# Performance work log

Hardware: AMD Instinct MI355X
Metric: run time of the kernel (lower is better)

## Reference

```python
import jax, jax.numpy as jnp
import numpy as np

EPS = 1e-5
N_HEADS = 8

def _layernorm(h, g, b):
    mu = jnp.mean(h, axis=-1, keepdims=True)
    var = jnp.mean((h - mu) ** 2, axis=-1, keepdims=True)
    return g * (h - mu) * jax.lax.rsqrt(var + EPS) + b

def _mlp_ln(x, W1, b1, W2, b2, g, beta):
    # Linear -> SiLU -> Linear -> LayerNorm (torch nn.Sequential processor)
    h = jax.nn.silu(x @ W1.T + b1)
    h = h @ W2.T + b2
    return _layernorm(h, g, beta)

def setup_inputs() -> dict:
    key = jax.random.key(0)
    ks = jax.random.split(key, 16)
    B, S, D = 4, 2048, 1024
    M, P, C = 128, 256, 512
    def lin(k, o, i):
        return (jax.random.normal(k, (o, i), jnp.float32) / np.sqrt(i)).astype(jnp.float32)
    inp = {}
    inp['x'] = jax.random.normal(ks[0], (B, S, D), jnp.float32)
    inp['scale_types'] = jax.random.randint(ks[1], (B, S), 0, 3)
    for name, dim, k1, k2 in [('mol', M, 2, 3), ('path', P, 4, 5), ('cell', C, 6, 7)]:
        inp[name + '_W1'] = lin(ks[k1], dim, D)
        inp[name + '_b1'] = jnp.zeros((dim,), jnp.float32)
        inp[name + '_W2'] = lin(ks[k2], dim, dim)
        inp[name + '_b2'] = jnp.zeros((dim,), jnp.float32)
        inp[name + '_g'] = jnp.ones((dim,), jnp.float32)
        inp[name + '_beta'] = jnp.zeros((dim,), jnp.float32)
    inp['int_W1'] = lin(ks[8], D, M + P + C)
    inp['int_b1'] = jnp.zeros((D,), jnp.float32)
    inp['int_W2'] = lin(ks[9], D, D)
    inp['int_b2'] = jnp.zeros((D,), jnp.float32)
    inp['int_g'] = jnp.ones((D,), jnp.float32)
    inp['int_beta'] = jnp.zeros((D,), jnp.float32)
    inp['attn_Wqkv'] = lin(ks[10], 3 * D, D)
    inp['attn_bqkv'] = jnp.zeros((3 * D,), jnp.float32)
    inp['attn_Wo'] = lin(ks[11], D, D)
    inp['attn_bo'] = jnp.zeros((D,), jnp.float32)
    inp['scale_w'] = jnp.ones((3,), jnp.float32) / 3.0
    return inp

def reference(x, scale_types,
              mol_W1, mol_b1, mol_W2, mol_b2, mol_g, mol_beta,
              path_W1, path_b1, path_W2, path_b2, path_g, path_beta,
              cell_W1, cell_b1, cell_W2, cell_b2, cell_g, cell_beta,
              int_W1, int_b1, int_W2, int_b2, int_g, int_beta,
              attn_Wqkv, attn_bqkv, attn_Wo, attn_bo, scale_w):
    B, S, D = x.shape
    # per-token routing: each token goes through exactly one expert; the
    # other two scale outputs are zeros (mask instead of Python loop).
    mol = _mlp_ln(x, mol_W1, mol_b1, mol_W2, mol_b2, mol_g, mol_beta) * (scale_types == 0)[..., None]
    path = _mlp_ln(x, path_W1, path_b1, path_W2, path_b2, path_g, path_beta) * (scale_types == 1)[..., None]
    cell = _mlp_ln(x, cell_W1, cell_b1, cell_W2, cell_b2, cell_g, cell_beta) * (scale_types == 2)[..., None]
    cat = jnp.concatenate([mol, path, cell], axis=-1)  # [B,S,M+P+C]
    integrated = _layernorm(jax.nn.silu(cat @ int_W1.T + int_b1) @ int_W2.T + int_b2, int_g, int_beta)
    # torch nn.MultiheadAttention (batch_first, self-attention)
    Dh = D // N_HEADS
    qkv = integrated @ attn_Wqkv.T + attn_bqkv  # [B,S,3D]
    q, k, v = jnp.split(qkv, 3, axis=-1)
    q = q.reshape(B, S, N_HEADS, Dh)
    k = k.reshape(B, S, N_HEADS, Dh)
    v = v.reshape(B, S, N_HEADS, Dh)
    scores = jnp.einsum('bqhd,bkhd->bhqk', q, k) / np.sqrt(Dh).astype(np.float32)
    attn = jax.nn.softmax(scores, axis=-1)
    o = jnp.einsum('bhqk,bkhd->bqhd', attn, v).reshape(B, S, D)
    attended = o @ attn_Wo.T + attn_bo
    w = jax.nn.softmax(scale_w, axis=0)
    final = integrated + w[0] * attended
    return (final, mol, path, cell)
```

## Files before the change

kernel.cpp:

```cpp
#include <hip/hip_runtime.h>
#include <cstdint>
#include <cstddef>

typedef unsigned short u16;
typedef unsigned int u32;
typedef short bf16x8 __attribute__((ext_vector_type(8)));
typedef float f32x4 __attribute__((ext_vector_type(4)));

__device__ __forceinline__ float bf2f(u16 u){
  union { u32 i; float f; } c; c.i = ((u32)u) << 16; return c.f;
}
__device__ __forceinline__ u16 f2bf(float f){
  union { float f; u32 i; } c; c.f = f;
  u32 r = c.i + 0x7FFFu + ((c.i >> 16) & 1u);
  return (u16)(r >> 16);
}
__device__ __forceinline__ void gload_lds16(const void* g, void* l){
  __builtin_amdgcn_global_load_lds(
      (const __attribute__((address_space(1))) u32*)g,
      (__attribute__((address_space(3))) u32*)l, 16, 0, 0);
}

struct ConvArgs {
  const float* src[11];
  u16* dst[11];
  u32 base[12];
  const float* b0; const float* b1; const float* b2;
  float* fbias;
};
__global__ __launch_bounds__(256)
void f32_to_bf16_multi(ConvArgs a){
  if (blockIdx.x == gridDim.x - 1){
    for (int i = threadIdx.x; i < 896; i += 256){
      float v;
      if (i < 128) v = a.b0[i];
      else if (i < 384) v = a.b1[i - 128];
      else v = a.b2[i - 384];
      a.fbias[i] = v;
    }
    return;
  }
  u32 i = blockIdx.x * 256 + threadIdx.x;
  if (i >= a.base[11]) return;
  int j = 0;
  #pragma unroll
  for (int k = 1; k < 11; ++k) j += (i >= a.base[k]);
  u32 li = i - a.base[j];
  const float4* s = (const float4*)a.src[j] + (size_t)li * 2;
  float4 va = s[0], vb = s[1];
  u16 o[8] = {f2bf(va.x),f2bf(va.y),f2bf(va.z),f2bf(va.w),
              f2bf(vb.x),f2bf(vb.y),f2bf(vb.z),f2bf(vb.w)};
  *(uint4*)(a.dst[j] + (size_t)li * 8) = *(const uint4*)o;
}

template<int EPI>
__device__ __forceinline__ void gemm_body(
    const u16* __restrict__ A, const u16* __restrict__ W,
    const float* __restrict__ bias, void* __restrict__ Cv,
    int N, int K, int lda, int ldc,
    const u16* __restrict__ I, const float* __restrict__ sw,
    int bx, int by)
{
  __shared__ __align__(16) u16 As[128*64];
  __shared__ __align__(16) u16 Bs[128*64];
  const int tid  = threadIdx.x;
  const int lane = tid & 63;
  const int wave = tid >> 6;
  const int wr = wave >> 1, wc = wave & 1;
  const int m0 = by * 128, n0 = bx * 128;

  f32x4 acc[4][4];
  #pragma unroll
  for (int r=0;r<4;++r)
    #pragma unroll
    for (int c=0;c<4;++c)
      #pragma unroll
      for (int e=0;e<4;++e) acc[r][c][e] = 0.f;

  int srow[4], soff[4];
  #pragma unroll
  for (int j=0;j<4;++j){
    int rr = (wave*4 + j)*8 + (lane>>3);
    srow[j] = rr;
    soff[j] = ((lane & 7) ^ (rr & 7)) * 8;
  }

  for (int k0 = 0; k0 < K; k0 += 64){
    #pragma unroll
    for (int j=0;j<4;++j){
      gload_lds16(A + (size_t)(m0 + srow[j])*lda + k0 + soff[j], As + (wave*4+j)*512);
      gload_lds16(W + (size_t)(n0 + srow[j])*K   + k0 + soff[j], Bs + (wave*4+j)*512);
    }
    __syncthreads();
    #pragma unroll
    for (int ks=0; ks<2; ++ks){
      bf16x8 af[4], bfr[4];
      #pragma unroll
      for (int r=0;r<4;++r){
        int row = wr*64 + r*16 + (lane&15);
        int cs  = (ks*4 + (lane>>4)) ^ (row & 7);
        af[r] = *(const bf16x8*)(As + row*64 + cs*8);
      }
      #pragma unroll
      for (int c=0;c<4;++c){
        int row = wc*64 + c*16 + (lane&15);
        int cs  = (ks*4 + (lane>>4)) ^ (row & 7);
        bfr[c] = *(const bf16x8*)(Bs + row*64 + cs*8);
      }
      #pragma unroll
      for (int r=0;r<4;++r)
        #pragma unroll
        for (int c=0;c<4;++c)
          acc[r][c] = __builtin_amdgcn_mfma_f32_16x16x32_bf16(af[r], bfr[c], acc[r][c], 0,0,0);
    }
    __syncthreads();
  }

  float w0 = 0.f;
  if (EPI == 2){
    float s0 = sw[0], s1 = sw[1], s2 = sw[2];
    float mx = fmaxf(s0, fmaxf(s1, s2));
    float e0 = __expf(s0-mx), e1 = __expf(s1-mx), e2 = __expf(s2-mx);
    w0 = e0 / (e0 + e1 + e2);
  }
  u16*   C16 = (u16*)Cv;
  float* C32 = (float*)Cv;
  #pragma unroll
  for (int c=0;c<4;++c){
    int col = n0 + wc*64 + c*16 + (lane&15);
    float bv = 0.f;
    size_t vtb = 0;
    if (EPI == 3){
      int tl = (col & 2047) >> 6, pos = col & 63;
      int p2 = pos & 31, hp = pos >> 5;
      int kap = hp*32 + (p2 < 16 ? 2*p2 : 2*(p2-16)+1);
      vtb = (size_t)(col >> 11) * 2097152 + (size_t)(tl*64 + kap);
    } else {
      bv = bias[col];
    }
    #pragma unroll
    for (int r=0;r<4;++r){
      int rbase = m0 + wr*64 + r*16 + (lane>>4)*4;
      #pragma unroll
      for (int e=0;e<4;++e){
        int row = rbase + e;
        float v = acc[r][c][e] + (EPI==3 ? bias[row] : bv);
        if (EPI == 1) v = v / (1.f + __expf(-v));
        if (EPI == 2){
          v = bf2f(I[(size_t)row*ldc + col]) + w0 * v;
          C32[(size_t)row*ldc + col] = v;
        } else if (EPI == 3){
          C16[vtb + (size_t)row*2048] = f2bf(v);
        } else {
          C16[(size_t)row*ldc + col] = f2bf(v);
        }
      }
    }
  }
}

template<int EPI>
__global__ __launch_bounds__(256, 4)
void gemm_bt(const u16* __restrict__ A, const u16* __restrict__ W,
             const float* __restrict__ bias, void* __restrict__ Cv,
             int N, int K, int lda, int ldc,
             const u16* __restrict__ I, const float* __restrict__ sw)
{
  gemm_body<EPI>(A, W, bias, Cv, N, K, lda, ldc, I, sw, blockIdx.x, blockIdx.y);
}

__global__ __launch_bounds__(256, 4)
void gemm_w2group(const u16* __restrict__ S1, u16* __restrict__ S2,
                  const u16* __restrict__ w0, const u16* __restrict__ w1,
                  const u16* __restrict__ w2, const float* __restrict__ b0,
                  const float* __restrict__ b1, const float* __restrict__ b2)
{
  int bx = blockIdx.x;
  if (bx < 64){
    gemm_body<0>(S1, w0, b0, S2, 128, 128, 896, 896, nullptr, nullptr, 0, bx);
  } else if (bx < 192){
    int l = bx - 64;
    gemm_body<0>(S1+128, w1, b1, S2+128, 256, 256, 896, 896, nullptr, nullptr, l>>6, l&63);
  } else {
    int l = bx - 192;
    gemm_body<0>(S1+384, w2, b2, S2+384, 512, 512, 896, 896, nullptr, nullptr, l>>6, l&63);
  }
}

__global__ __launch_bounds__(256, 4)
void gemm_qkv_vt(const u16* __restrict__ integ, const u16* __restrict__ Wqkv,
                 const float* __restrict__ bqkv, u16* __restrict__ qkv,
                 u16* __restrict__ vt)
{
  int bx = blockIdx.x;
  if (bx < 1024){
    gemm_body<0>(integ, Wqkv, bqkv, qkv, 2048, 1024, 1024, 3072,
                 nullptr, nullptr, bx & 15, bx >> 4);
  } else {
    int l = bx - 1024;
    gemm_body<3>(Wqkv + (size_t)2048*1024, integ, bqkv + 2048, vt, 8192, 1024,
                 1024, 2048, nullptr, nullptr, l & 63, l >> 6);
  }
}

template<int D>
__device__ __forceinline__ void ln_body_masked(
    u16* __restrict__ H, int ldh, const float* __restrict__ g,
    const float* __restrict__ beta, const int* __restrict__ st,
    int eid, float* __restrict__ outp)
{
  const int tid = threadIdx.x, lane = tid & 63, wave = tid >> 6;
  const int token = blockIdx.x * 4 + wave;
  constexpr int VPT = D / 64;
  float v[VPT];
  u16* row = H + (size_t)token * ldh + lane * VPT;
  #pragma unroll
  for (int i=0;i<VPT/2;++i){
    u32 u = ((const u32*)row)[i];
    v[2*i]   = bf2f((u16)(u & 0xFFFFu));
    v[2*i+1] = bf2f((u16)(u >> 16));
  }
  float s = 0.f;
  #pragma unroll
  for (int i=0;i<VPT;++i) s += v[i];
  #pragma unroll
  for (int off=1; off<64; off<<=1) s += __shfl_xor(s, off);
  float mu = s * (1.f / D);
  float q = 0.f;
  #pragma unroll
  for (int i=0;i<VPT;++i){ float d = v[i] - mu; q += d * d; }
  #pragma unroll
  for (int off=1; off<64; off<<=1) q += __shfl_xor(q, off);
  float rs = rsqrtf(q * (1.f / D) + 1e-5f);
  float msk = (st[token] == eid) ? 1.f : 0.f;
  #pragma unroll
  for (int i=0;i<VPT;++i){
    float gg = g[lane*VPT + i];
    float bb = beta[lane*VPT + i];
    float val = (gg * (v[i] - mu) * rs + bb) * msk;
    outp[(size_t)token * D + lane * VPT + i] = val;
    row[i] = f2bf(val);
  }
}

__global__ __launch_bounds__(256, 4)
void ln_expert(u16* __restrict__ S2,
               const float* __restrict__ g0, const float* __restrict__ be0,
               const float* __restrict__ g1, const float* __restrict__ be1,
               const float* __restrict__ g2, const float* __restrict__ be2,
               const int* __restrict__ st,
               float* __restrict__ o0, float* __restrict__ o1,
               float* __restrict__ o2)
{
  if (blockIdx.y == 0)      ln_body_masked<128>(S2,     896, g0, be0, st, 0, o0);
  else if (blockIdx.y == 1) ln_body_masked<256>(S2+128, 896, g1, be1, st, 1, o1);
  else                      ln_body_masked<512>(S2+384, 896, g2, be2, st, 2, o2);
}

__global__ __launch_bounds__(256, 4)
void ln_int(const u16* __restrict__ H, const float* __restrict__ g,
            const float* __restrict__ beta, u16* __restrict__ outp)
{
  const int tid = threadIdx.x, lane = tid & 63, wave = tid >> 6;
  const int token = blockIdx.x * 4 + wave;
  constexpr int D = 1024, VPT = 16;
  float v[VPT];
  const u16* row = H + (size_t)token * D + lane * VPT;
  #pragma unroll
  for (int i=0;i<VPT/2;++i){
    u32 u = ((const u32*)row)[i];
    v[2*i]   = bf2f((u16)(u & 0xFFFFu));
    v[2*i+1] = bf2f((u16)(u >> 16));
  }
  float s = 0.f;
  #pragma unroll
  for (int i=0;i<VPT;++i) s += v[i];
  #pragma unroll
  for (int off=1; off<64; off<<=1) s += __shfl_xor(s, off);
  float mu = s * (1.f / D);
  float q = 0.f;
  #pragma unroll
  for (int i=0;i<VPT;++i){ float d = v[i] - mu; q += d * d; }
  #pragma unroll
  for (int off=1; off<64; off<<=1) q += __shfl_xor(q, off);
  float rs = rsqrtf(q * (1.f / D) + 1e-5f);
  #pragma unroll
  for (int i=0;i<VPT;++i){
    float val = g[lane*VPT + i] * (v[i] - mu) * rs + beta[lane*VPT + i];
    outp[(size_t)token * D + lane * VPT + i] = f2bf(val);
  }
}

__global__ __launch_bounds__(256, 4)
void flash_attn(const u16* __restrict__ qkv, const u16* __restrict__ vt,
                u16* __restrict__ o)
{
  __shared__ __align__(16) u16 Ks[8192];
  __shared__ __align__(16) u16 Vs[8192];
  __shared__ __align__(16) u16 Ps[4*1024];
  const int tid = threadIdx.x, lane = tid & 63, wave = tid >> 6;
  const int b = blockIdx.z, h = blockIdx.y, q0 = blockIdx.x * 64;
  const float cl2   = 0.12751791892f;
  const float DEFER = 90.50966799187809f;

  bf16x8 qreg[4];
  {
    const u16* qrow = qkv + (size_t)(b*2048 + q0 + wave*16 + (lane&15))*3072
                      + h*128 + (lane>>4)*8;
    #pragma unroll
    for (int kk=0;kk<4;++kk) qreg[kk] = *(const bf16x8*)(qrow + kk*32);
  }
  asm volatile("s_waitcnt vmcnt(0)" ::: "memory");

  const u16* ksrc[4]; const u16* vsrc[4]; int cdst[4];
  #pragma unroll
  for (int i=0;i<4;++i){
    int cidx = (wave*4 + i)*64 + lane;
    int krow = cidx >> 4, kcs = cidx & 15;
    int kcsrc = (kcs & 8) | ((kcs & 7) ^ (krow & 7));
    ksrc[i] = qkv + (size_t)(b*2048 + krow)*3072 + h*128 + 1024 + kcsrc*8;
    int vd = cidx >> 3, vcs = cidx & 7;
    vsrc[i] = vt + ((size_t)(b*8 + h)*128 + vd)*2048 + (vcs ^ (vd & 7))*8;
    cdst[i] = cidx * 8;
  }

  int koff[16];
  #pragma unroll
  for (int kk=0;kk<4;++kk)
    #pragma unroll
    for (int cb=0;cb<4;++cb){
      int row  = (lane&15) + 16*cb;
      int c    = kk*4 + (lane>>4);
      int slot = (c & 8) | ((c & 7) ^ (row & 7));
      koff[kk*4+cb] = (row*128 + slot*8) * 2;
    }
  int voff[16];
  #pragma unroll
  for (int kk=0;kk<2;++kk)
    #pragma unroll
    for (int f=0;f<8;++f){
      int d = f*16 + (lane&15);
      int c = kk*4 + (lane>>4);
      voff[kk*8+f] = (d*64 + (c ^ (d & 7))*8) * 2;
    }
  int pwoff[8];
  #pragma unroll
  for (int e=0;e<4;++e){
    int prow = (lane>>4)*4 + e;
    int j01 = lane & 15;
    int j23 = 16 + (lane & 15);
    pwoff[e*2]   = (prow*32 + (((((j01>>2) ^ (prow&7)) & 7)<<2) | (j01&3))) * 4;
    pwoff[e*2+1] = (prow*32 + (((((j23>>2) ^ (prow&7)) & 7)<<2) | (j23&3))) * 4;
  }
  int proff[2];
  #pragma unroll
  for (int kk=0;kk<2;++kk){
    int prow = lane & 15;
    int pc   = kk*4 + (lane>>4);
    proff[kk] = (prow*64 + ((pc ^ (prow & 7)) & 7)*8) * 2;
  }

  auto stageK = [&](){
    #pragma unroll
    for (int i=0;i<4;++i){ gload_lds16(ksrc[i], Ks + cdst[i]); ksrc[i] += 196608; }
  };
  auto stageV = [&](){
    #pragma unroll
    for (int i=0;i<4;++i){ gload_lds16(vsrc[i], Vs + cdst[i]); vsrc[i] += 64; }
  };

  f32x4 oacc[8];
  #pragma unroll
  for (int f=0;f<8;++f)
    #pragma unroll
    for (int e=0;e<4;++e) oacc[f][e] = 0.f;
  float m_run[4] = {-3e38f,-3e38f,-3e38f,-3e38f};
  float l_run[4] = {0.f,0.f,0.f,0.f};
  const char* KsB = (const char*)Ks;
  const char* VsB = (const char*)Vs;
  char* PsWB = (char*)(Ps + wave*1024);

  stageK();
  stageV();
  asm volatile("s_waitcnt vmcnt(4)" ::: "memory");
  __builtin_amdgcn_s_barrier();
  __builtin_amdgcn_sched_barrier(0);

  for (int kt=0; kt<32; ++kt){
    f32x4 s[4];
    #pragma unroll
    for (int cb=0;cb<4;++cb)
      #pragma unroll
      for (int e=0;e<4;++e) s[cb][e] = 0.f;
    __builtin_amdgcn_s_setprio(1);
    #pragma unroll
    for (int kk=0;kk<4;++kk){
      #pragma unroll
      for (int cb=0;cb<4;++cb){
        bf16x8 bk = *(const bf16x8*)(KsB + koff[kk*4+cb]);
        s[cb] = __builtin_amdgcn_mfma_f32_16x16x32_bf16(qreg[kk], bk, s[cb], 0,0,0);
      }
    }
    __builtin_amdgcn_s_setprio(0);
    asm volatile("s_waitcnt lgkmcnt(0)" ::: "memory");
    __builtin_amdgcn_sched_barrier(0);
    __builtin_amdgcn_s_barrier();
    __builtin_amdgcn_sched_barrier(0);
    stageK();

    #pragma unroll
    for (int e=0;e<4;++e){
      float t0 = s[0][e], t1 = s[1][e], t2 = s[2][e], t3 = s[3][e];
      float lmx = fmaxf(fmaxf(t0,t1), fmaxf(t2,t3));
      if (__any(lmx > m_run[e] + DEFER)){
        float mx = lmx;
        #pragma unroll
        for (int off=1; off<16; off<<=1) mx = fmaxf(mx, __shfl_xor(mx, off));
        float mnew = fmaxf(m_run[e], mx);
        float a = exp2f((m_run[e] - mnew) * cl2);
        m_run[e] = mnew;
        l_run[e] *= a;
        #pragma unroll
        for (int f=0;f<8;++f) oacc[f][e] *= a;
      }
      float ms = m_run[e];
      float p0 = exp2f((t0 - ms)*cl2), p1 = exp2f((t1 - ms)*cl2);
      float p2 = exp2f((t2 - ms)*cl2), p3 = exp2f((t3 - ms)*cl2);
      l_run[e] += (p0 + p1) + (p2 + p3);
      u32 c01, c23;
      asm("v_cvt_pk_bf16_f32 %0, %1, %2" : "=v"(c01) : "v"(p0), "v"(p1));
      asm("v_cvt_pk_bf16_f32 %0, %1, %2" : "=v"(c23) : "v"(p2), "v"(p3));
      *(u32*)(PsWB + pwoff[e*2])   = c01;
      *(u32*)(PsWB + pwoff[e*2+1]) = c23;
    }

    asm volatile("s_waitcnt vmcnt(4)" ::: "memory");
    __builtin_amdgcn_sched_barrier(0);
    __builtin_amdgcn_s_barrier();
    __builtin_amdgcn_sched_barrier(0);

    __builtin_amdgcn_s_setprio(1);
    #pragma unroll
    for (int kk=0;kk<2;++kk){
      bf16x8 pa = *(const bf16x8*)(PsWB + proff[kk]);
      #pragma unroll
      for (int f=0;f<8;++f){
        bf16x8 vb = *(const bf16x8*)(VsB + voff[kk*8+f]);
        oacc[f] = __builtin_amdgcn_mfma_f32_16x16x32_bf16(pa, vb, oacc[f], 0,0,0);
      }
    }
    __builtin_amdgcn_s_setprio(0);
    asm volatile("s_waitcnt lgkmcnt(0) vmcnt(0)" ::: "memory");
    __builtin_amdgcn_sched_barrier(0);
    __builtin_amdgcn_s_barrier();
    __builtin_amdgcn_sched_barrier(0);
    if (kt + 1 < 32) stageV();
  }

  #pragma unroll
  for (int e=0;e<4;++e){
    float l = l_run[e];
    #pragma unroll
    for (int off=1; off<16; off<<=1) l += __shfl_xor(l, off);
    l_run[e] = 1.f / l;
  }
  #pragma unroll
  for (int f=0;f<8;++f)
    #pragma unroll
    for (int e=0;e<4;++e){
      int row = q0 + wave*16 + (lane>>4)*4 + e;
      int col = h*128 + f*16 + (lane&15);
      o[(size_t)(b*2048 + row)*1024 + col] = f2bf(oacc[f][e] * l_run[e]);
    }
}

extern "C" void kernel_launch(void* const* d_in, const int* in_sizes, int n_in,
                              void* d_out, int out_size, void* d_ws, size_t ws_size,
                              hipStream_t stream)
{
  const float* x         = (const float*)d_in[0];
  const int*   stypes    = (const int*)d_in[1];
  const float* mol_W1    = (const float*)d_in[2];
  const float* mol_b1    = (const float*)d_in[3];
  const float* mol_W2    = (const float*)d_in[4];
  const float* mol_b2    = (const float*)d_in[5];
  const float* mol_g     = (const float*)d_in[6];
  const float* mol_beta  = (const float*)d_in[7];
  const float* path_W1   = (const float*)d_in[8];
  const float* path_b1   = (const float*)d_in[9];
  const float* path_W2   = (const float*)d_in[10];
  const float* path_b2   = (const float*)d_in[11];
  const float* path_g    = (const float*)d_in[12];
  const float* path_beta = (const float*)d_in[13];
  const float* cell_W1   = (const float*)d_in[14];
  const float* cell_b1   = (const float*)d_in[15];
  const float* cell_W2   = (const float*)d_in[16];
  const float* cell_b2   = (const float*)d_in[17];
  const float* cell_g    = (const float*)d_in[18];
  const float* cell_beta = (const float*)d_in[19];
  const float* int_W1    = (const float*)d_in[20];
  const float* int_b1    = (const float*)d_in[21];
  const float* int_W2    = (const float*)d_in[22];
  const float* int_b2    = (const float*)d_in[23];
  const float* int_g     = (const float*)d_in[24];
  const float* int_beta  = (const float*)d_in[25];
  const float* attn_Wqkv = (const float*)d_in[26];
  const float* attn_bqkv = (const float*)d_in[27];
  const float* attn_Wo   = (const float*)d_in[28];
  const float* attn_bo   = (const float*)d_in[29];
  const float* scale_w   = (const float*)d_in[30];

  float* out_final = (float*)d_out;
  float* out_mol   = out_final + 8388608;
  float* out_path  = out_mol   + 1048576;
  float* out_cell  = out_path  + 2097152;

  u16* ws    = (u16*)d_ws;
  u16* qkv   = ws;
  u16* integ = qkv   + 25165824;
  u16* S1    = integ + 8388608;
  u16* S2    = S1    + 8388608;
  u16* wb    = S2    + 8388608;
  u16* xb    = qkv;

  u16* w1f    = wb;
  u16* molW2b = w1f    + 917504;
  u16* pathW2b= molW2b + 16384;
  u16* cellW2b= pathW2b+ 65536;
  u16* intW1b = cellW2b+ 262144;
  u16* intW2b = intW1b + 917504;
  u16* qkvWb  = intW2b + 1048576;
  u16* woWb   = qkvWb  + 3145728;
  float* fbias= (float*)(woWb + 1048576);

  dim3 blk(256);

  ConvArgs ca;
  const float* srcs[11] = {x, mol_W1, path_W1, cell_W1, mol_W2, path_W2,
                           cell_W2, int_W1, int_W2, attn_Wqkv, attn_Wo};
  u16* dsts[11] = {xb, w1f, w1f + 131072, w1f + 393216, molW2b, pathW2b,
                   cellW2b, intW1b, intW2b, qkvWb, woWb};
  u32 n8s[11] = {1048576, 16384, 32768, 65536, 2048, 8192,
                 32768, 114688, 131072, 393216, 131072};
  u32 acc8 = 0;
  for (int i=0;i<11;++i){ ca.src[i]=srcs[i]; ca.dst[i]=dsts[i]; ca.base[i]=acc8; acc8+=n8s[i]; }
  ca.base[11] = acc8;
  ca.b0 = mol_b1; ca.b1 = path_b1; ca.b2 = cell_b1; ca.fbias = fbias;
  f32_to_bf16_multi<<<(acc8 + 255)/256 + 1, blk, 0, stream>>>(ca);

  gemm_bt<1><<<dim3(7,64), blk, 0, stream>>>(xb, w1f, fbias, S1, 896, 1024, 1024, 896, nullptr, nullptr);
  gemm_w2group<<<448, blk, 0, stream>>>(S1, S2, molW2b, pathW2b, cellW2b,
                                        mol_b2, path_b2, cell_b2);
  ln_expert<<<dim3(2048,3), blk, 0, stream>>>(S2, mol_g, mol_beta, path_g,
                                              path_beta, cell_g, cell_beta,
                                              stypes, out_mol, out_path, out_cell);

  gemm_bt<1><<<dim3(8,64), blk, 0, stream>>>(S2, intW1b, int_b1, S1, 1024, 896,  896,  1024, nullptr, nullptr);
  gemm_bt<0><<<dim3(8,64), blk, 0, stream>>>(S1, intW2b, int_b2, S2, 1024, 1024, 1024, 1024, nullptr, nullptr);
  ln_int<<<2048, blk, 0, stream>>>(S2, int_g, int_beta, integ);

  gemm_qkv_vt<<<1536, blk, 0, stream>>>(integ, qkvWb, attn_bqkv, qkv, S2);
  flash_attn<<<dim3(32,8,4), blk, 0, stream>>>(qkv, S2, S1);

  gemm_bt<2><<<dim3(8,64), blk, 0, stream>>>(S1, woWb, attn_bo, out_final, 1024, 1024, 1024, 1024, integ, scale_w);
}
```

Before: 327.7 us.

## Add triple-buffered 256x128-tile GEMM with async LDS staging for large GEMMs

Adds a new GEMM path that uses 512-thread blocks computing 256x128 tiles. It stages A and W tiles into a three-slot LDS ring with global_load_lds, waits with explicit vmcnt counts and raises wave priority around the MFMA loop, so global loads overlap compute instead of being fully serialized by barriers. The epilogue is split into a shared helper. The first expert GEMM, both integration GEMMs, QKV/V-transpose and output projection switch to it with halved grids. The cost is about 147KB of LDS per block, which allows only one block per CU, and grids of 224–256 blocks that may underfill the device.

Result: no change. 323.7 us (-1.2%).

```diff
diff --git a/kernel.cpp b/kernel.cpp
--- a/kernel.cpp
+++ b/kernel.cpp
@@ -54,68 +54,10 @@
 }
 
 template<int EPI>
-__device__ __forceinline__ void gemm_body(
-    const u16* __restrict__ A, const u16* __restrict__ W,
-    const float* __restrict__ bias, void* __restrict__ Cv,
-    int N, int K, int lda, int ldc,
-    const u16* __restrict__ I, const float* __restrict__ sw,
-    int bx, int by)
-{
-  __shared__ __align__(16) u16 As[128*64];
-  __shared__ __align__(16) u16 Bs[128*64];
-  const int tid  = threadIdx.x;
-  const int lane = tid & 63;
-  const int wave = tid >> 6;
-  const int wr = wave >> 1, wc = wave & 1;
-  const int m0 = by * 128, n0 = bx * 128;
-
-  f32x4 acc[4][4];
-  #pragma unroll
-  for (int r=0;r<4;++r)
-    #pragma unroll
-    for (int c=0;c<4;++c)
-      #pragma unroll
-      for (int e=0;e<4;++e) acc[r][c][e] = 0.f;
-
-  int srow[4], soff[4];
-  #pragma unroll
-  for (int j=0;j<4;++j){
-    int rr = (wave*4 + j)*8 + (lane>>3);
-    srow[j] = rr;
-    soff[j] = ((lane & 7) ^ (rr & 7)) * 8;
-  }
-
-  for (int k0 = 0; k0 < K; k0 += 64){
-    #pragma unroll
-    for (int j=0;j<4;++j){
-      gload_lds16(A + (size_t)(m0 + srow[j])*lda + k0 + soff[j], As + (wave*4+j)*512);
-      gload_lds16(W + (size_t)(n0 + srow[j])*K   + k0 + soff[j], Bs + (wave*4+j)*512);
-    }
-    __syncthreads();
-    #pragma unroll
-    for (int ks=0; ks<2; ++ks){
-      bf16x8 af[4], bfr[4];
-      #pragma unroll
-      for (int r=0;r<4;++r){
-        int row = wr*64 + r*16 + (lane&15);
-        int cs  = (ks*4 + (lane>>4)) ^ (row & 7);
-        af[r] = *(const bf16x8*)(As + row*64 + cs*8);
-      }
-      #pragma unroll
-      for (int c=0;c<4;++c){
-        int row = wc*64 + c*16 + (lane&15);
-        int cs  = (ks*4 + (lane>>4)) ^ (row & 7);
-        bfr[c] = *(const bf16x8*)(Bs + row*64 + cs*8);
-      }
-      #pragma unroll
-      for (int r=0;r<4;++r)
-        #pragma unroll
-        for (int c=0;c<4;++c)
-          acc[r][c] = __builtin_amdgcn_mfma_f32_16x16x32_bf16(af[r], bfr[c], acc[r][c], 0,0,0);
-    }
-    __syncthreads();
-  }
-
+__device__ __forceinline__ void gemm_epilogue(
+    f32x4 acc[4][4], const float* bias, void* Cv, int N, int ldc,
+    const u16* I, const float* sw, int m0, int n0, int wr, int wc, int lane)
+{
   float w0 = 0.f;
   if (EPI == 2){
     float s0 = sw[0], s1 = sw[1], s2 = sw[2];
@@ -160,13 +102,68 @@
 }
 
 template<int EPI>
-__global__ __launch_bounds__(256, 4)
-void gemm_bt(const u16* __restrict__ A, const u16* __restrict__ W,
-             const float* __restrict__ bias, void* __restrict__ Cv,
-             int N, int K, int lda, int ldc,
-             const u16* __restrict__ I, const float* __restrict__ sw)
-{
-  gemm_body<EPI>(A, W, bias, Cv, N, K, lda, ldc, I, sw, blockIdx.x, blockIdx.y);
+__device__ __forceinline__ void gemm_body(
+    const u16* __restrict__ A, const u16* __restrict__ W,
+    const float* __restrict__ bias, void* __restrict__ Cv,
+    int N, int K, int lda, int ldc,
+    const u16* __restrict__ I, const float* __restrict__ sw,
+    int bx, int by)
+{
+  __shared__ __align__(16) u16 As[128*64];
+  __shared__ __align__(16) u16 Bs[128*64];
+  const int tid  = threadIdx.x;
+  const int lane = tid & 63;
+  const int wave = tid >> 6;
+  const int wr = wave >> 1, wc = wave & 1;
+  const int m0 = by * 128, n0 = bx * 128;
+
+  f32x4 acc[4][4];
+  #pragma unroll
+  for (int r=0;r<4;++r)
+    #pragma unroll
+    for (int c=0;c<4;++c)
+      #pragma unroll
+      for (int e=0;e<4;++e) acc[r][c][e] = 0.f;
+
+  int srow[4], soff[4];
+  #pragma unroll
+  for (int j=0;j<4;++j){
+    int rr = (wave*4 + j)*8 + (lane>>3);
+    srow[j] = rr;
+    soff[j] = ((lane & 7) ^ (rr & 7)) * 8;
+  }
+
+  for (int k0 = 0; k0 < K; k0 += 64){
+    #pragma unroll
+    for (int j=0;j<4;++j){
+      gload_lds16(A + (size_t)(m0 + srow[j])*lda + k0 + soff[j], As + (wave*4+j)*512);
+      gload_lds16(W + (size_t)(n0 + srow[j])*K   + k0 + soff[j], Bs + (wave*4+j)*512);
+    }
+    __syncthreads();
+    #pragma unroll
+    for (int ks=0; ks<2; ++ks){
+      bf16x8 af[4], bfr[4];
+      #pragma unroll
+      for (int r=0;r<4;++r){
+        int row = wr*64 + r*16 + (lane&15);
+        int cs  = (ks*4 + (lane>>4)) ^ (row & 7);
+        af[r] = *(const bf16x8*)(As + row*64 + cs*8);
+      }
+      #pragma unroll
+      for (int c=0;c<4;++c){
+        int row = wc*64 + c*16 + (lane&15);
+        int cs  = (ks*4 + (lane>>4)) ^ (row & 7);
+        bfr[c] = *(const bf16x8*)(Bs + row*64 + cs*8);
+      }
+      #pragma unroll
+      for (int r=0;r<4;++r)
+        #pragma unroll
+        for (int c=0;c<4;++c)
+          acc[r][c] = __builtin_amdgcn_mfma_f32_16x16x32_bf16(af[r], bfr[c], acc[r][c], 0,0,0);
+    }
+    __syncthreads();
+  }
+  gemm_epilogue<EPI>(acc, bias, Cv, N, ldc, I, sw, m0, n0, wr, wc, lane);
 }
 
 __global__ __launch_bounds__(256, 4)
@@ -187,19 +184,116 @@
   }
 }
 
-__global__ __launch_bounds__(256, 4)
-void gemm_qkv_vt(const u16* __restrict__ integ, const u16* __restrict__ Wqkv,
-                 const float* __restrict__ bqkv, u16* __restrict__ qkv,
-                 u16* __restrict__ vt)
-{
+template<int EPI>
+__device__ __forceinline__ void gemm_body2(
+    u16* __restrict__ S,
+    const u16* __restrict__ A, const u16* __restrict__ W,
+    const float* __restrict__ bias, void* __restrict__ Cv,
+    int N, int K, int lda, int ldc,
+    const u16* __restrict__ I, const float* __restrict__ sw,
+    int bx, int by)
+{
+  const int tid = threadIdx.x, lane = tid & 63, wave = tid >> 6;
+  const int wr = wave >> 1, wc = wave & 1;
+  const int m0 = by * 256, n0 = bx * 128;
+
+  f32x4 acc[4][4];
+  #pragma unroll
+  for (int r=0;r<4;++r)
+    #pragma unroll
+    for (int c=0;c<4;++c)
+      #pragma unroll
+      for (int e=0;e<4;++e) acc[r][c][e] = 0.f;
+
+  const u16* src[6]; int dst6[6];
+  #pragma unroll
+  for (int i=0;i<6;++i){
+    int c = i*512 + tid;
+    int row = c >> 3, slot = c & 7;
+    int soff = (slot ^ (row & 7)) * 8;
+    src[i] = (row < 256) ? A + (size_t)(m0 + row)*lda + soff
+                         : W + (size_t)(n0 + row - 256)*K + soff;
+    dst6[i] = c * 8;
+  }
+  const int nt = K >> 6;
+  auto stage = [&](int buf, int kt){
+    u16* base = S + buf*24576;
+    #pragma unroll
+    for (int i=0;i<6;++i) gload_lds16(src[i] + kt*64, base + dst6[i]);
+  };
+
+  stage(0, 0);
+  stage(1, 1);
+  asm volatile("s_waitcnt vmcnt(6)" ::: "memory");
+  __builtin_amdgcn_s_barrier();
+  __builtin_amdgcn_sched_barrier(0);
+
+  int cur = 0;
+  for (int t = 0; t < nt; ++t){
+    int nxt = (t + 2 < nt) ? t + 2 : nt - 1;
+    int sb = cur + 2; if (sb >= 3) sb -= 3;
+    stage(sb, nxt);
+
+    const u16* As = S + cur*24576;
+    const u16* Bs = As + 16384;
+    __builtin_amdgcn_s_setprio(1);
+    #pragma unroll
+    for (int ks=0; ks<2; ++ks){
+      bf16x8 af[4], bfr[4];
+      #pragma unroll
+      for (int r=0;r<4;++r){
+        int row = wr*64 + r*16 + (lane&15);
+        int cs  = (ks*4 + (lane>>4)) ^ (row & 7);
+        af[r] = *(const bf16x8*)(As + row*64 + cs*8);
+      }
+      #pragma unroll
+      for (int c=0;c<4;++c){
+        int row = wc*64 + c*16 + (lane&15);
+        int cs  = (ks*4 + (lane>>4)) ^ (row & 7);
+        bfr[c] = *(const bf16x8*)(Bs + row*64 + cs*8);
+      }
+      #pragma unroll
+      for (int r=0;r<4;++r)
+        #pragma unroll
+        for (int c=0;c<4;++c)
+          acc[r][c] = __builtin_amdgcn_mfma_f32_16x16x32_bf16(af[r], bfr[c], acc[r][c], 0,0,0);
+    }
+    __builtin_amdgcn_s_setprio(0);
+    asm volatile("s_waitcnt vmcnt(6)" ::: "memory");
+    __builtin_amdgcn_sched_barrier(0);
+    __builtin_amdgcn_s_barrier();
+    __builtin_amdgcn_sched_barrier(0);
+    cur += 1; if (cur >= 3) cur -= 3;
+  }
+
+  gemm_epilogue<EPI>(acc, bias, Cv, N, ldc, I, sw, m0, n0, wr, wc, lane);
+}
+
+template<int EPI>
+__global__ __launch_bounds__(512, 1)
+void gemm_bt2(const u16* __restrict__ A, const u16* __restrict__ W,
+              const float* __restrict__ bias, void* __restrict__ Cv,
+              int N, int K, int lda, int ldc,
+              const u16* __restrict__ I, const float* __restrict__ sw)
+{
+  __shared__ __align__(16) u16 S[3*24576];
+  gemm_body2<EPI>(S, A, W, bias, Cv, N, K, lda, ldc, I, sw, blockIdx.x, blockIdx.y);
+}
+
+__global__ __launch_bounds__(512, 1)
+void gemm_qkv_vt2(const u16* __restrict__ integ, const u16* __restrict__ Wqkv,
+                  const float* __restrict__ bqkv, u16* __restrict__ qkv,
+                  u16* __restrict__ vt)
+{
+  __shared__ __align__(16) u16 S[3*24576];
   int bx = blockIdx.x;
-  if (bx < 1024){
-    gemm_body<0>(integ, Wqkv, bqkv, qkv, 2048, 1024, 1024, 3072,
-                 nullptr, nullptr, bx & 15, bx >> 4);
+  if (bx < 512){
+    gemm_body2<0>(S, integ, Wqkv, bqkv, qkv, 2048, 1024, 1024, 3072,
+                  nullptr, nullptr, bx & 15, bx >> 4);
   } else {
-    int l = bx - 1024;
-    gemm_body<3>(Wqkv + (size_t)2048*1024, integ, bqkv + 2048, vt, 8192, 1024,
-                 1024, 2048, nullptr, nullptr, l & 63, l >> 6);
+    int l = bx - 512;
+    gemm_body2<3>(S, Wqkv + (size_t)2048*1024, integ, bqkv + 2048, vt, 8192, 1024,
+                  1024, 2048, nullptr, nullptr, l & 63, l >> 6);
   }
 }
 
@@ -534,6 +628,7 @@
   float* fbias= (float*)(woWb + 1048576);
 
   dim3 blk(256);
+  dim3 blk2(512);
 
   ConvArgs ca;
   const float* srcs[11] = {x, mol_W1, path_W1, cell_W1, mol_W2, path_W2,
@@ -548,19 +643,19 @@
   ca.b0 = mol_b1; ca.b1 = path_b1; ca.b2 = cell_b1; ca.fbias = fbias;
   f32_to_bf16_multi<<<(acc8 + 255)/256 + 1, blk, 0, stream>>>(ca);
 
-  gemm_bt<1><<<dim3(7,64), blk, 0, stream>>>(xb, w1f, fbias, S1, 896, 1024, 1024, 896, nullptr, nullptr);
+  gemm_bt2<1><<<dim3(7,32), blk2, 0, stream>>>(xb, w1f, fbias, S1, 896, 1024, 1024, 896, nullptr, nullptr);
   gemm_w2group<<<448, blk, 0, stream>>>(S1, S2, molW2b, pathW2b, cellW2b,
                                         mol_b2, path_b2, cell_b2);
   ln_expert<<<dim3(2048,3), blk, 0, stream>>>(S2, mol_g, mol_beta, path_g,
                                               path_beta, cell_g, cell_beta,
                                               stypes, out_mol, out_path, out_cell);
 
-  gemm_bt<1><<<dim3(8,64), blk, 0, stream>>>(S2, intW1b, int_b1, S1, 1024, 896,  896,  1024, nullptr, nullptr);
-  gemm_bt<0><<<dim3(8,64), blk, 0, stream>>>(S1, intW2b, int_b2, S2, 1024, 1024, 1024, 1024, nullptr, nullptr);
+  gemm_bt2<1><<<dim3(8,32), blk2, 0, stream>>>(S2, intW1b, int_b1, S1, 1024, 896,  896,  1024, nullptr, nullptr);
+  gemm_bt2<0><<<dim3(8,32), blk2, 0, stream>>>(S1, intW2b, int_b2, S2, 1024, 1024, 1024, 1024, nullptr, nullptr);
   ln_int<<<2048, blk, 0, stream>>>(S2, int_g, int_beta, integ);
 
-  gemm_qkv_vt<<<1536, blk, 0, stream>>>(integ, qkvWb, attn_bqkv, qkv, S2);
+  gemm_qkv_vt2<<<768, blk2, 0, stream>>>(integ, qkvWb, attn_bqkv, qkv, S2);
   flash_attn<<<dim3(32,8,4), blk, 0, stream>>>(qkv, S2, S1);
 
-  gemm_bt<2><<<dim3(8,64), blk, 0, stream>>>(S1, woWb, attn_bo, out_final, 1024, 1024, 1024, 1024, integ, scale_w);
-}
+  gemm_bt2<2><<<dim3(8,32), blk2, 0, stream>>>(S1, woWb, attn_bo, out_final, 1024, 1024, 1024, 1024, integ, scale_w);
+}
```
